# Optimization experiments

Measured on AMD Instinct MI355X. Metric: run time of the kernel, lower is better.

## Reference

```python
import jax, jax.numpy as jnp
import numpy as np

N_NODES = 100000
N_EDGES = 1600000
D_IN = 64
D_OUT = 64


def setup_inputs() -> dict:
    key = jax.random.key(0)
    k1, k2, k3 = jax.random.split(key, 3)
    edge_index = jax.random.randint(k1, (2, N_EDGES), 0, N_NODES, dtype=jnp.int64)
    x = jax.random.normal(k2, (N_NODES, D_IN), dtype=jnp.float32)
    W = jax.random.normal(k3, (D_OUT, D_IN), dtype=jnp.float32) * (1.0 / np.sqrt(D_IN))
    return {"edge_index": edge_index, "x": x, "W": W}


def reference(edge_index, x, W):
    # GCN forward: h = W x, then out = D^{-1/2} A D^{-1/2} h (symmetric normalization
    # of the COO edge list, matching normalize_edge_index + CSR SpMM in the original).
    N = x.shape[0]
    row, col = edge_index[0], edge_index[1]
    # degree from row occurrences of the adjacency
    deg = jax.ops.segment_sum(jnp.ones(row.shape, x.dtype), row, num_segments=N)
    dinv_sqrt = jnp.where(deg > 0, 1.0 / jnp.sqrt(deg), 0.0)
    w = dinv_sqrt[row] * dinv_sqrt[col]  # [E] edge weights
    xh = x @ W.T                          # dense linear, bias=False  [N, D_OUT]
    # SpMM: out[r] = sum_e w_e * xh[col_e] for edges with row_e == r
    out = jax.ops.segment_sum(w[:, None] * xh[col], row, num_segments=N)
    return out
```

## Files before the change

kernel.cpp:

```cpp
#include <hip/hip_runtime.h>
#include <hip/hip_fp16.h>

#define D     64
#define RPB   256
#define BCAP  4608
#define EPB   4096
#define NBMAX 400

typedef __attribute__((ext_vector_type(8))) _Float16 f16x8;
typedef __attribute__((ext_vector_type(4))) float    f32x4;

__global__ __launch_bounds__(512) void bucket_kernel(const int* __restrict__ ei, int E,
                                                     int nb,
                                                     int* __restrict__ cursor,
                                                     int* __restrict__ bbuf) {
    __shared__ int hist[NBMAX];
    __shared__ int base_l[NBMAX];
    int tid = threadIdx.x;

    for (int i = tid; i < nb; i += 512) hist[i] = 0;
    __syncthreads();

    int e0 = blockIdx.x * EPB;
    int n  = min(EPB, E - e0);

    for (int idx = tid; idx < n; idx += 512)
        atomicAdd(&hist[ei[e0 + idx] >> 8], 1);
    __syncthreads();

    for (int i = tid; i < nb; i += 512) {
        int c = hist[i];
        base_l[i] = (c > 0) ? atomicAdd(&cursor[i], c) : 0;
        hist[i] = 0;
    }
    __syncthreads();

    for (int idx = tid; idx < n; idx += 512) {
        int r = ei[e0 + idx];
        int c = ei[E + e0 + idx];
        int b = r >> 8;
        int off = base_l[b] + atomicAdd(&hist[b], 1);
        if (off < BCAP)
            bbuf[(size_t)b * BCAP + off] = ((r & (RPB - 1)) << 17) | c;
    }
}

__global__ __launch_bounds__(512) void sort_linear_kernel(const int* __restrict__ cursor,
                                                          int* __restrict__ bbuf,
                                                          const float* __restrict__ x,
                                                          const float* __restrict__ W,
                                                          int4* __restrict__ rowinfo,
                                                          __half* __restrict__ xh, int N) {
    __shared__ int   sorted[BCAP];
    __shared__ int   hist[RPB];
    __shared__ int   curs[RPB];
    __shared__ float sdinv[RPB];
    __shared__ int   wsum[4];
    int b = blockIdx.x, tid = threadIdx.x;
    int cnt = min(cursor[b], BCAP);
    int* gbuf = bbuf + (size_t)b * BCAP;

    if (tid < RPB) hist[tid] = 0;
    __syncthreads();

    for (int j = tid * 4; j < cnt; j += 2048) {
        int4 v = *(const int4*)(gbuf + j);
        atomicAdd(&hist[(v.x >> 17) & 255], 1);
        if (j + 1 < cnt) atomicAdd(&hist[(v.y >> 17) & 255], 1);
        if (j + 2 < cnt) atomicAdd(&hist[(v.z >> 17) & 255], 1);
        if (j + 3 < cnt) atomicAdd(&hist[(v.w >> 17) & 255], 1);
    }
    __syncthreads();

    int dv = 0, s = 0;
    if (tid < RPB) {
        dv = hist[tid];
        s = dv;
#pragma unroll
        for (int off = 1; off < 64; off <<= 1) {
            int t = __shfl_up(s, off);
            if ((tid & 63) >= off) s += t;
        }
        if ((tid & 63) == 63) wsum[tid >> 6] = s;
    }
    __syncthreads();
    if (tid < RPB) {
        int woff = 0;
#pragma unroll
        for (int i = 0; i < 3; ++i)
            if ((tid >> 6) > i) woff += wsum[i];
        int excl = s + woff - dv;
        float di = (dv > 0) ? rsqrtf((float)dv) : 0.0f;
        sdinv[tid] = di;
        int r = (b << 8) + tid;
        if (r < N)
            rowinfo[r] = make_int4(b * BCAP + excl, dv, __float_as_int(di), 0);
        curs[tid] = excl;
    }
    __syncthreads();

    for (int j = tid * 4; j < cnt; j += 2048) {
        int4 v = *(const int4*)(gbuf + j);
        sorted[atomicAdd(&curs[(v.x >> 17) & 255], 1)] = v.x;
        if (j + 1 < cnt) sorted[atomicAdd(&curs[(v.y >> 17) & 255], 1)] = v.y;
        if (j + 2 < cnt) sorted[atomicAdd(&curs[(v.z >> 17) & 255], 1)] = v.z;
        if (j + 3 < cnt) sorted[atomicAdd(&curs[(v.w >> 17) & 255], 1)] = v.w;
    }
    __syncthreads();

    int cnt4 = (cnt + 3) & ~3;
    for (int j = tid * 4; j < cnt4; j += 2048)
        *(int4*)(gbuf + j) = *(const int4*)(sorted + j);

    int lane = tid & 63;
    int wv   = tid >> 6;
    int r16  = lane & 15;
    int quad = lane >> 4;

    if (b == 0 && tid < D) xh[(size_t)N * D + tid] = __float2half(0.0f);

    f16x8 Bf[4][2];
#pragma unroll
    for (int g = 0; g < 4; ++g)
#pragma unroll
        for (int s2 = 0; s2 < 2; ++s2) {
            const float4* wp = (const float4*)(W + (size_t)(16 * g + r16) * D + 32 * s2 + quad * 8);
            float4 w0 = wp[0], w1 = wp[1];
            f16x8 h;
            h[0] = (_Float16)w0.x; h[1] = (_Float16)w0.y;
            h[2] = (_Float16)w0.z; h[3] = (_Float16)w0.w;
            h[4] = (_Float16)w1.x; h[5] = (_Float16)w1.y;
            h[6] = (_Float16)w1.z; h[7] = (_Float16)w1.w;
            Bf[g][s2] = h;
        }

    for (int tl = wv; tl < 16; tl += 8) {
        int r0 = (b << 8) + tl * 16;
        if (r0 >= N) break;
        int ra = min(r0 + r16, N - 1);
        const float4* xp = (const float4*)(x + (size_t)ra * D + quad * 8);
        float4 a0 = xp[0], a1 = xp[1], a2 = xp[8], a3 = xp[9];
        f16x8 A0, A1;
        A0[0] = (_Float16)a0.x; A0[1] = (_Float16)a0.y; A0[2] = (_Float16)a0.z; A0[3] = (_Float16)a0.w;
        A0[4] = (_Float16)a1.x; A0[5] = (_Float16)a1.y; A0[6] = (_Float16)a1.z; A0[7] = (_Float16)a1.w;
        A1[0] = (_Float16)a2.x; A1[1] = (_Float16)a2.y; A1[2] = (_Float16)a2.z; A1[3] = (_Float16)a2.w;
        A1[4] = (_Float16)a3.x; A1[5] = (_Float16)a3.y; A1[6] = (_Float16)a3.z; A1[7] = (_Float16)a3.w;

        f32x4 acc[4];
#pragma unroll
        for (int g = 0; g < 4; ++g) {
            f32x4 z = {0.f, 0.f, 0.f, 0.f};
            z = __builtin_amdgcn_mfma_f32_16x16x32_f16(A0, Bf[g][0], z, 0, 0, 0);
            acc[g] = __builtin_amdgcn_mfma_f32_16x16x32_f16(A1, Bf[g][1], z, 0, 0, 0);
        }

#pragma unroll
        for (int reg = 0; reg < 4; ++reg) {
            int rl = tl * 16 + quad * 4 + reg;
            int rr = (b << 8) + rl;
            if (rr < N) {
                float dvr = sdinv[rl];
                __half* op = xh + (size_t)rr * D + r16;
#pragma unroll
                for (int g = 0; g < 4; ++g)
                    op[16 * g] = __float2half(dvr * acc[g][reg]);
            }
        }
    }
}

__global__ __launch_bounds__(256) void spmm_kernel(const int4* __restrict__ rowinfo,
                                                   const int* __restrict__ bbuf,
                                                   const float2* __restrict__ xhq,
                                                   float4* __restrict__ out4,
                                                   int N, int stride) {
    int wid = (blockIdx.x * 256 + threadIdx.x) >> 6;
    int c   = threadIdx.x & 63;
    int sub = c >> 4;
    int f   = c & 15;

    int r0 = wid;
    if (r0 >= N) return;

    int4 ri0 = rowinfo[r0];
    int4 ri1 = (r0 + stride < N) ? rowinfo[r0 + stride] : make_int4(0, 0, 0, 0);
    int  cn0 = (c < min(ri0.y, 64)) ? (bbuf[ri0.x + c] & 0x1FFFF) : N;

    for (int r = r0; r < N; r += stride) {
        int rn  = r + stride;
        int rn2 = rn + stride;
        int4 ri2 = (rn2 < N) ? rowinfo[rn2] : make_int4(0, 0, 0, 0);
        int  cn1 = (rn < N && c < min(ri1.y, 64)) ? (bbuf[ri1.x + c] & 0x1FFFF) : N;

        int   d  = ri0.y;
        float dr = __int_as_float(ri0.z);
        float a0 = 0.f, a1 = 0.f, a2 = 0.f, a3 = 0.f;

        int n = min(d, 64);
        int n16 = (n + 15) & ~15;
        for (int k = 0; k < n16; k += 16) {
            int e0 = __shfl(cn0, k +  0 + sub);
            int e1 = __shfl(cn0, k +  4 + sub);
            int e2 = __shfl(cn0, k +  8 + sub);
            int e3 = __shfl(cn0, k + 12 + sub);
            float2 q0 = xhq[(size_t)e0 * 16 + f];
            float2 q1 = xhq[(size_t)e1 * 16 + f];
            float2 q2 = xhq[(size_t)e2 * 16 + f];
            float2 q3 = xhq[(size_t)e3 * 16 + f];
            float2 u;
            u = __half22float2(__builtin_bit_cast(__half2, q0.x)); a0 += u.x; a1 += u.y;
            u = __half22float2(__builtin_bit_cast(__half2, q0.y)); a2 += u.x; a3 += u.y;
            u = __half22float2(__builtin_bit_cast(__half2, q1.x)); a0 += u.x; a1 += u.y;
            u = __half22float2(__builtin_bit_cast(__half2, q1.y)); a2 += u.x; a3 += u.y;
            u = __half22float2(__builtin_bit_cast(__half2, q2.x)); a0 += u.x; a1 += u.y;
            u = __half22float2(__builtin_bit_cast(__half2, q2.y)); a2 += u.x; a3 += u.y;
            u = __half22float2(__builtin_bit_cast(__half2, q3.x)); a0 += u.x; a1 += u.y;
            u = __half22float2(__builtin_bit_cast(__half2, q3.y)); a2 += u.x; a3 += u.y;
        }
        for (int j0 = 64; j0 < d; j0 += 64) {
            int nn = min(d - j0, 64);
            int cnx = (c < nn) ? (bbuf[ri0.x + j0 + c] & 0x1FFFF) : N;
            int m16 = (nn + 15) & ~15;
            for (int k = 0; k < m16; k += 16) {
                int e0 = __shfl(cnx, k +  0 + sub);
                int e1 = __shfl(cnx, k +  4 + sub);
                int e2 = __shfl(cnx, k +  8 + sub);
                int e3 = __shfl(cnx, k + 12 + sub);
                float2 q0 = xhq[(size_t)e0 * 16 + f];
                float2 q1 = xhq[(size_t)e1 * 16 + f];
                float2 q2 = xhq[(size_t)e2 * 16 + f];
                float2 q3 = xhq[(size_t)e3 * 16 + f];
                float2 u;
                u = __half22float2(__builtin_bit_cast(__half2, q0.x)); a0 += u.x; a1 += u.y;
                u = __half22float2(__builtin_bit_cast(__half2, q0.y)); a2 += u.x; a3 += u.y;
                u = __half22float2(__builtin_bit_cast(__half2, q1.x)); a0 += u.x; a1 += u.y;
                u = __half22float2(__builtin_bit_cast(__half2, q1.y)); a2 += u.x; a3 += u.y;
                u = __half22float2(__builtin_bit_cast(__half2, q2.x)); a0 += u.x; a1 += u.y;
                u = __half22float2(__builtin_bit_cast(__half2, q2.y)); a2 += u.x; a3 += u.y;
                u = __half22float2(__builtin_bit_cast(__half2, q3.x)); a0 += u.x; a1 += u.y;
                u = __half22float2(__builtin_bit_cast(__half2, q3.y)); a2 += u.x; a3 += u.y;
            }
        }

        float t0 = a0 + __shfl(a0, c ^ 16);
        float t1 = a1 + __shfl(a1, c ^ 16);
        float t2 = a2 + __shfl(a2, c ^ 16);
        float t3 = a3 + __shfl(a3, c ^ 16);
        float s0 = t0 + __shfl(t0, c ^ 32);
        float s1 = t1 + __shfl(t1, c ^ 32);
        float s2 = t2 + __shfl(t2, c ^ 32);
        float s3 = t3 + __shfl(t3, c ^ 32);
        if (sub == 0) {
            f32x4 res = {dr * s0, dr * s1, dr * s2, dr * s3};
            __builtin_nontemporal_store(res, (f32x4*)&out4[(size_t)r * 16 + f]);
        }
        ri0 = ri1; ri1 = ri2; cn0 = cn1;
    }
}

extern "C" void kernel_launch(void* const* d_in, const int* in_sizes, int n_in,
                              void* d_out, int out_size, void* d_ws, size_t ws_size,
                              hipStream_t stream) {
    const int*   ei = (const int*)d_in[0];
    const float* x  = (const float*)d_in[1];
    const float* W  = (const float*)d_in[2];
    float* out = (float*)d_out;

    int E  = in_sizes[0] / 2;
    int N  = in_sizes[1] / D;
    int nb = (N + RPB - 1) / RPB;

    char* p = (char*)d_ws;
    size_t off = 0;
    auto take = [&](size_t bytes) -> char* {
        char* cur = p + off;
        off = (off + bytes + 255) & ~(size_t)255;
        return cur;
    };
    int4*   rowinfo = (int4*)take((size_t)N * 16);
    int*    cursor  = (int*)take((size_t)nb * 4);
    int*    bbuf    = (int*)take((size_t)nb * BCAP * 4);
    __half* xh      = (__half*)take((size_t)(N + 1) * D * 2);
    (void)ws_size;

    hipMemsetAsync(cursor, 0, (size_t)nb * 4, stream);

    bucket_kernel<<<(E + EPB - 1) / EPB, 512, 0, stream>>>(ei, E, nb, cursor, bbuf);
    sort_linear_kernel<<<nb, 512, 0, stream>>>(cursor, bbuf, x, W, rowinfo, xh, N);

    int spmm_blocks = 3072;
    spmm_kernel<<<spmm_blocks, 256, 0, stream>>>(rowinfo, bbuf, (const float2*)xh,
                                                 (float4*)out, N, spmm_blocks * 4);
}
```

Baseline: 161.5 us.

## Assign one 16-lane group per row in SpMM instead of one wavefront

The SpMM kernel now maps each output row to a 16-lane group rather than a full 64-lane wavefront, so four rows are processed per wavefront. Each group loads 16 neighbour indices at a time, shuffles them within the group, and issues 16 independent gathers before accumulating, which removes the cross-sub-wave reduction shuffles. It also drops the software prefetch of the next row's metadata. The intent is better lane utilisation for average degree around 16 and more memory-level parallelism, at the cost of divergence when rows in the same wavefront have different degrees.

After: 161.1 us. Within noise of the previous version (-0.3%).

```diff
diff --git a/kernel.cpp b/kernel.cpp
--- a/kernel.cpp
+++ b/kernel.cpp
@@ -173,88 +173,37 @@
                                                    const int* __restrict__ bbuf,
                                                    const float2* __restrict__ xhq,
                                                    float4* __restrict__ out4,
-                                                   int N, int stride) {
-    int wid = (blockIdx.x * 256 + threadIdx.x) >> 6;
-    int c   = threadIdx.x & 63;
-    int sub = c >> 4;
-    int f   = c & 15;
-
-    int r0 = wid;
-    if (r0 >= N) return;
-
-    int4 ri0 = rowinfo[r0];
-    int4 ri1 = (r0 + stride < N) ? rowinfo[r0 + stride] : make_int4(0, 0, 0, 0);
-    int  cn0 = (c < min(ri0.y, 64)) ? (bbuf[ri0.x + c] & 0x1FFFF) : N;
-
-    for (int r = r0; r < N; r += stride) {
-        int rn  = r + stride;
-        int rn2 = rn + stride;
-        int4 ri2 = (rn2 < N) ? rowinfo[rn2] : make_int4(0, 0, 0, 0);
-        int  cn1 = (rn < N && c < min(ri1.y, 64)) ? (bbuf[ri1.x + c] & 0x1FFFF) : N;
-
-        int   d  = ri0.y;
-        float dr = __int_as_float(ri0.z);
+                                                   int N, int ngroups) {
+    int gid = (blockIdx.x * 256 + threadIdx.x) >> 4;
+    int l   = threadIdx.x & 15;
+    int gq  = (threadIdx.x >> 4) & 3;
+
+    for (int r = gid; r < N; r += ngroups) {
+        int4  ri    = rowinfo[r];
+        int   start = ri.x, deg = ri.y;
+        float dr    = __int_as_float(ri.z);
         float a0 = 0.f, a1 = 0.f, a2 = 0.f, a3 = 0.f;
 
-        int n = min(d, 64);
-        int n16 = (n + 15) & ~15;
-        for (int k = 0; k < n16; k += 16) {
-            int e0 = __shfl(cn0, k +  0 + sub);
-            int e1 = __shfl(cn0, k +  4 + sub);
-            int e2 = __shfl(cn0, k +  8 + sub);
-            int e3 = __shfl(cn0, k + 12 + sub);
-            float2 q0 = xhq[(size_t)e0 * 16 + f];
-            float2 q1 = xhq[(size_t)e1 * 16 + f];
-            float2 q2 = xhq[(size_t)e2 * 16 + f];
-            float2 q3 = xhq[(size_t)e3 * 16 + f];
-            float2 u;
-            u = __half22float2(__builtin_bit_cast(__half2, q0.x)); a0 += u.x; a1 += u.y;
-            u = __half22float2(__builtin_bit_cast(__half2, q0.y)); a2 += u.x; a3 += u.y;
-            u = __half22float2(__builtin_bit_cast(__half2, q1.x)); a0 += u.x; a1 += u.y;
-            u = __half22float2(__builtin_bit_cast(__half2, q1.y)); a2 += u.x; a3 += u.y;
-            u = __half22float2(__builtin_bit_cast(__half2, q2.x)); a0 += u.x; a1 += u.y;
-            u = __half22float2(__builtin_bit_cast(__half2, q2.y)); a2 += u.x; a3 += u.y;
-            u = __half22float2(__builtin_bit_cast(__half2, q3.x)); a0 += u.x; a1 += u.y;
-            u = __half22float2(__builtin_bit_cast(__half2, q3.y)); a2 += u.x; a3 += u.y;
-        }
-        for (int j0 = 64; j0 < d; j0 += 64) {
-            int nn = min(d - j0, 64);
-            int cnx = (c < nn) ? (bbuf[ri0.x + j0 + c] & 0x1FFFF) : N;
-            int m16 = (nn + 15) & ~15;
-            for (int k = 0; k < m16; k += 16) {
-                int e0 = __shfl(cnx, k +  0 + sub);
-                int e1 = __shfl(cnx, k +  4 + sub);
-                int e2 = __shfl(cnx, k +  8 + sub);
-                int e3 = __shfl(cnx, k + 12 + sub);
-                float2 q0 = xhq[(size_t)e0 * 16 + f];
-                float2 q1 = xhq[(size_t)e1 * 16 + f];
-                float2 q2 = xhq[(size_t)e2 * 16 + f];
-                float2 q3 = xhq[(size_t)e3 * 16 + f];
-                float2 u;
-                u = __half22float2(__builtin_bit_cast(__half2, q0.x)); a0 += u.x; a1 += u.y;
-                u = __half22float2(__builtin_bit_cast(__half2, q0.y)); a2 += u.x; a3 += u.y;
-                u = __half22float2(__builtin_bit_cast(__half2, q1.x)); a0 += u.x; a1 += u.y;
-                u = __half22float2(__builtin_bit_cast(__half2, q1.y)); a2 += u.x; a3 += u.y;
-                u = __half22float2(__builtin_bit_cast(__half2, q2.x)); a0 += u.x; a1 += u.y;
-                u = __half22float2(__builtin_bit_cast(__half2, q2.y)); a2 += u.x; a3 += u.y;
-                u = __half22float2(__builtin_bit_cast(__half2, q3.x)); a0 += u.x; a1 += u.y;
-                u = __half22float2(__builtin_bit_cast(__half2, q3.y)); a2 += u.x; a3 += u.y;
+        for (int j0 = 0; j0 < deg; j0 += 16) {
+            int nn = deg - j0;
+            int cn = (l < nn) ? (bbuf[start + j0 + l] & 0x1FFFF) : N;
+
+            float2 q[16];
+#pragma unroll
+            for (int k = 0; k < 16; ++k) {
+                int e = __shfl(cn, (gq << 4) + k);
+                q[k] = xhq[(size_t)e * 16 + l];
             }
-        }
-
-        float t0 = a0 + __shfl(a0, c ^ 16);
-        float t1 = a1 + __shfl(a1, c ^ 16);
-        float t2 = a2 + __shfl(a2, c ^ 16);
-        float t3 = a3 + __shfl(a3, c ^ 16);
-        float s0 = t0 + __shfl(t0, c ^ 32);
-        float s1 = t1 + __shfl(t1, c ^ 32);
-        float s2 = t2 + __shfl(t2, c ^ 32);
-        float s3 = t3 + __shfl(t3, c ^ 32);
-        if (sub == 0) {
-            f32x4 res = {dr * s0, dr * s1, dr * s2, dr * s3};
-            __builtin_nontemporal_store(res, (f32x4*)&out4[(size_t)r * 16 + f]);
-        }
-        ri0 = ri1; ri1 = ri2; cn0 = cn1;
+#pragma unroll
+            for (int k = 0; k < 16; ++k) {
+                float2 u0 = __half22float2(__builtin_bit_cast(__half2, q[k].x));
+                float2 u1 = __half22float2(__builtin_bit_cast(__half2, q[k].y));
+                a0 += u0.x; a1 += u0.y; a2 += u1.x; a3 += u1.y;
+            }
+        }
+
+        f32x4 res = {dr * a0, dr * a1, dr * a2, dr * a3};
+        __builtin_nontemporal_store(res, (f32x4*)&out4[(size_t)r * 16 + l]);
     }
 }
 
@@ -290,5 +239,5 @@
 
     int spmm_blocks = 3072;
     spmm_kernel<<<spmm_blocks, 256, 0, stream>>>(rowinfo, bbuf, (const float2*)xh,
-                                                 (float4*)out, N, spmm_blocks * 4);
-}
+                                                 (float4*)out, N, spmm_blocks * 16);
+}
```
